# Optimization experiments

Measured on AMD Instinct MI355X. Metric: run time of the kernel, lower is better.

The kernel has to match this reference:

```python
import jax, jax.numpy as jnp
from jax import lax
import numpy as np

D_MODEL = 1024
D_STATE = 16
D_CONV = 4
EXPAND = 2
D_INNER = EXPAND * D_MODEL  # 2048
DT_RANK = D_MODEL // 16     # 64
BATCH = 4
SEQ = 1024


def setup_inputs() -> dict:
    key = jax.random.key(0)
    ks = iter(jax.random.split(key, 40))
    def w(shape, s=0.02):
        return (s * jax.random.normal(next(ks), shape)).astype(jnp.float32)
    inp = {"x": jax.random.normal(next(ks), (BATCH, SEQ, D_MODEL), dtype=jnp.float32)}
    # S4D-real style A init: A = -exp(A_log), A_log = log(1..N) per channel
    Alog = jnp.log(jnp.tile(jnp.arange(1, D_STATE + 1, dtype=jnp.float32), (D_INNER, 1)))
    for s in ("f", "b"):
        inp[f"inproj_{s}"] = w((D_MODEL, 2 * D_INNER))
        inp[f"conv_w_{s}"] = w((D_INNER, D_CONV), 0.2)
        inp[f"conv_b_{s}"] = jnp.zeros((D_INNER,), jnp.float32)
        inp[f"xproj_{s}"] = w((D_INNER, DT_RANK + 2 * D_STATE))
        inp[f"dt_w_{s}"] = w((DT_RANK, D_INNER))
        inp[f"dt_b_{s}"] = jnp.full((D_INNER,), -4.0, jnp.float32)  # softplus(-4)~0.018
        inp[f"Alog_{s}"] = Alog
        inp[f"Dp_{s}"] = jnp.ones((D_INNER,), jnp.float32)
        inp[f"outproj_{s}"] = w((D_INNER, D_MODEL))
    inp["gate_w"] = w((2 * D_MODEL, D_MODEL))
    inp["gate_b"] = jnp.zeros((D_MODEL,), jnp.float32)
    inp["proj_w"] = w((D_MODEL, D_MODEL))
    inp["proj_b"] = jnp.zeros((D_MODEL,), jnp.float32)
    return inp


def _mamba(x, inproj, conv_w, conv_b, xproj, dt_w, dt_b, Alog, Dp, outproj):
    B, L, _ = x.shape
    xz = x @ inproj                           # [B,L,2*Di]
    u, z = jnp.split(xz, 2, axis=-1)          # each [B,L,Di]
    # depthwise causal conv1d, width D_CONV
    K = conv_w.shape[1]
    up = jnp.pad(u, ((0, 0), (K - 1, 0), (0, 0)))
    uc = conv_b
    for k in range(K):
        uc = uc + up[:, k:k + L, :] * conv_w[:, k]
    uc = jax.nn.silu(uc)                      # [B,L,Di]
    dbl = uc @ xproj                          # [B,L,dt_rank+2N]
    N = Alog.shape[1]
    dt, Bm, Cm = jnp.split(dbl, [DT_RANK, DT_RANK + N], axis=-1)
    delta = jax.nn.softplus(dt @ dt_w + dt_b) # [B,L,Di]
    A = -jnp.exp(Alog)                        # [Di,N]

    def step(h, inp):
        u_t, d_t, B_t, C_t = inp              # [B,Di],[B,Di],[B,N],[B,N]
        dA = jnp.exp(d_t[..., None] * A)      # [B,Di,N]
        h = dA * h + (d_t * u_t)[..., None] * B_t[:, None, :]
        y_t = jnp.einsum('bdn,bn->bd', h, C_t)
        return h, y_t

    h0 = jnp.zeros((B, uc.shape[-1], N), x.dtype)
    xs = (uc.transpose(1, 0, 2), delta.transpose(1, 0, 2),
          Bm.transpose(1, 0, 2), Cm.transpose(1, 0, 2))
    _, ys = lax.scan(step, h0, xs)            # ys: [L,B,Di]
    y = ys.transpose(1, 0, 2) + uc * Dp
    y = y * jax.nn.silu(z)
    return y @ outproj                        # [B,L,d_model]


def reference(x, inproj_f, conv_w_f, conv_b_f, xproj_f, dt_w_f, dt_b_f, Alog_f, Dp_f, outproj_f,
              inproj_b, conv_w_b, conv_b_b, xproj_b, dt_w_b, dt_b_b, Alog_b, Dp_b, outproj_b,
              gate_w, gate_b, proj_w, proj_b):
    y_f = _mamba(x, inproj_f, conv_w_f, conv_b_f, xproj_f, dt_w_f, dt_b_f, Alog_f, Dp_f, outproj_f)
    xb = jnp.flip(x, axis=1)
    y_b = _mamba(xb, inproj_b, conv_w_b, conv_b_b, xproj_b, dt_w_b, dt_b_b, Alog_b, Dp_b, outproj_b)
    y_b = jnp.flip(y_b, axis=1)
    g = jax.nn.sigmoid(jnp.concatenate([y_f, y_b], axis=-1) @ gate_w + gate_b)
    y = g * y_f + (1.0 - g) * y_b
    return y @ proj_w + proj_b
```

## Files before the change

kernel.cpp:

```cpp
#include <hip/hip_runtime.h>
#include <hip/hip_bf16.h>

#define B_  4
#define L_  1024
#define DM  1024
#define DI  2048
#define NS  16
#define RK  64
#define MT  (B_ * L_)
#define NC  32
#define CH  (L_ / NC)
#define KSX 256
#define NZX 8
#define PSZ (B_ * NC * NS * DI)

typedef unsigned short u16;
typedef __attribute__((ext_vector_type(8))) short  bh8;
typedef __attribute__((ext_vector_type(8))) unsigned short us8;
typedef __attribute__((ext_vector_type(8))) _Float16 h8;
typedef __attribute__((ext_vector_type(4))) float  f4;

__device__ __forceinline__ float bf2f(u16 u) {
  union { unsigned int i; float f; } c; c.i = ((unsigned int)u) << 16; return c.f;
}
__device__ __forceinline__ u16 f2bf(float f) {
  union { float f; unsigned int i; } c; c.f = f;
  unsigned int x = c.i;
  unsigned int r = (x + 0x7fffu + ((x >> 16) & 1u)) >> 16;
  return (u16)r;
}

__device__ __forceinline__ void gl16(const u16* g, u16* l) {
  __builtin_amdgcn_global_load_lds(
      (const __attribute__((address_space(1))) void*)g,
      (__attribute__((address_space(3))) void*)l, 16, 0, 0);
}

__global__ void detect_k(const unsigned int* __restrict__ alog,
                         int* __restrict__ flag, int* __restrict__ afl) {
  *flag = (alog[0] != 0u) ? 1 : 0;
  afl[0] = 1; afl[1] = 1;
}

__global__ __launch_bounds__(256)
void cvt_k(const void* __restrict__ src, u16* __restrict__ dst, int n,
           const int* __restrict__ flag) {
  int i = blockIdx.x * 256 + threadIdx.x;
  if (i >= n) return;
  if (*flag) dst[i] = ((const u16*)src)[i];
  else       dst[i] = f2bf(((const float*)src)[i]);
}

__global__ __launch_bounds__(256)
void cvt10_k(const int* __restrict__ flagp,
             const void* s0, u16* d0, int n0, const void* s1, u16* d1, int n1,
             const void* s2, u16* d2, int n2, const void* s3, u16* d3, int n3,
             const void* s4, u16* d4, int n4, const void* s5, u16* d5, int n5,
             const void* s6, u16* d6, int n6, const void* s7, u16* d7, int n7,
             const void* s8, u16* d8, int n8, const void* s9, u16* d9, int n9)
{
  const void* s; u16* d; int n;
  switch (blockIdx.y) {
    case 0: s = s0; d = d0; n = n0; break;  case 1: s = s1; d = d1; n = n1; break;
    case 2: s = s2; d = d2; n = n2; break;  case 3: s = s3; d = d3; n = n3; break;
    case 4: s = s4; d = d4; n = n4; break;  case 5: s = s5; d = d5; n = n5; break;
    case 6: s = s6; d = d6; n = n6; break;  case 7: s = s7; d = d7; n = n7; break;
    case 8: s = s8; d = d8; n = n8; break;  default: s = s9; d = d9; n = n9; break;
  }
  int i = blockIdx.x * 256 + threadIdx.x;
  if (i >= n) return;
  d[i] = *flagp ? ((const u16*)s)[i] : f2bf(((const float*)s)[i]);
}

__global__ __launch_bounds__(256)
void a2_k(const int* __restrict__ flagp, const void* __restrict__ sf,
          const void* __restrict__ sb, _Float16* __restrict__ A2h,
          int* __restrict__ afl)
{
  int i = blockIdx.x * 256 + threadIdx.x;
  int dir = i >> 15;
  const void* src = dir ? sb : sf;
  int j = i & (DI * NS - 1);
  float v = *flagp ? bf2f(((const u16*)src)[j]) : ((const float*)src)[j];
  float a2 = -__expf(v);
  A2h[i] = (_Float16)a2;
  int n = i & 15;
  if (fabsf(a2 + (float)(n + 1)) > 1e-3f * (n + 1)) atomicAnd(&afl[dir], 0);
}

struct TpBatch {
  const void* src[8];
  u16* dst[8];
  int R[8], C[8], tilesX[8];
  int tOff[9];
  int cnt;
};

__global__ __launch_bounds__(256)
void tposeB_k(TpBatch tb, const int* __restrict__ flag) {
  __shared__ u16 tile[32][33];
  int bid = blockIdx.x;
  int i = 0;
  #pragma unroll
  for (int q = 0; q < 7; ++q) if (i + 1 < tb.cnt && bid >= tb.tOff[i + 1]) ++i;
  int local = bid - tb.tOff[i];
  int tX = tb.tilesX[i];
  int c0 = (local % tX) * 32, r0 = (local / tX) * 32;
  int R = tb.R[i], C = tb.C[i];
  const void* src = tb.src[i];
  u16* dst = tb.dst[i];
  int tx = threadIdx.x & 31, ty = threadIdx.x >> 5;
  int isbf = *flag;
  #pragma unroll
  for (int k = 0; k < 4; ++k) {
    int r = r0 + ty + k * 8, c = c0 + tx;
    u16 v = 0;
    if (r < R && c < C)
      v = isbf ? ((const u16*)src)[(size_t)r * C + c]
               : f2bf(((const float*)src)[(size_t)r * C + c]);
    tile[ty + k * 8][tx] = v;
  }
  __syncthreads();
  #pragma unroll
  for (int k = 0; k < 4; ++k) {
    int c = c0 + ty + k * 8, r = r0 + tx;
    if (c < C && r < R)
      dst[(size_t)c * R + r] = tile[tx][ty + k * 8];
  }
}

template<int ACT, int CATM, int OUTF, int BIDIR, int SPLITK, int DUO, int XSW, int ZDIR>
__global__ __launch_bounds__(256)
void gemm2(const u16* __restrict__ A, int lda,
           const u16* __restrict__ Wt,
           const u16* __restrict__ bias,
           void* __restrict__ Cp, int ldc, void* __restrict__ C2,
           int M, int N, int K,
           const u16* __restrict__ yfp, const u16* __restrict__ ybp,
           const int* __restrict__ flagp, const u16* __restrict__ Aalt)
{
  __shared__ __align__(16) u16 As[128][64];
  __shared__ __align__(16) u16 Bs[128][64];

  int bx, by;
  if (XSW) {
    int g = blockIdx.y * gridDim.x + blockIdx.x;
    int xcd = g & 7, j = g >> 3;
    int bxb = gridDim.x >> 3;
    int sh = 31 - __builtin_clz(bxb);
    bx = xcd * bxb + (j & (bxb - 1));
    by = j >> sh;
  } else { bx = blockIdx.x; by = blockIdx.y; }

  int zdir = 0, zslice = 0;
  if (ZDIR && SPLITK) { zdir = blockIdx.z >> 3; zslice = blockIdx.z & (NZX - 1); }
  else if (ZDIR)      { zdir = blockIdx.z; }
  else if (SPLITK)    { zslice = blockIdx.z; }

  const int tid  = threadIdx.x;
  const int lane = tid & 63;
  const int w    = tid >> 6;
  const int wm   = (w >> 1) * 64, wn = (w & 1) * 64;
  const int bm0  = by * 128, bn0 = bx * 128;
  const int l15  = lane & 15, quad = lane >> 4;
  const int rI8  = lane >> 3;
  const int cG8  = (lane & 7) ^ rI8;

  const u16* Wtp = ZDIR ? (Wt + (size_t)zdir * N * K) : Wt;

  f4 acc[4][4] = {};

  const int kb = SPLITK ? zslice * KSX : 0;
  const int ke = SPLITK ? kb + KSX : K;

  for (int k0 = kb; k0 < ke; k0 += 64) {
    {
      const u16* Abase;
      if (ZDIR)     Abase = zdir ? Aalt : A;
      else if (DUO) Abase = (bn0 < DM) ? A : ybp;
      else          Abase = A;
      #pragma unroll
      for (int t = 0; t < 4; ++t) {
        int rb = w * 32 + t * 8;
        int row = rb + rI8;
        const u16* gp;
        if (CATM) {
          int kk = k0 + cG8 * 8;
          int m = bm0 + row;
          gp = (kk < DM) ? (yfp + (size_t)m * DM + kk)
                         : (ybp + (size_t)(m ^ (L_ - 1)) * DM + (kk - DM));
        } else {
          gp = Abase + (size_t)(bm0 + row) * lda + k0 + cG8 * 8;
        }
        gl16(gp, &As[rb][0]);
      }
    }
    #pragma unroll
    for (int t = 0; t < 4; ++t) {
      int rb = w * 32 + t * 8;
      int row = rb + rI8;
      int n = bn0 + row; if (n > N - 1) n = N - 1;
      gl16(Wtp + (size_t)n * K + k0 + cG8 * 8, &Bs[rb][0]);
    }
    __syncthreads();
    #pragma unroll
    for (int s = 0; s < 2; ++s) {
      bh8 af[4], bg[4];
      const int phys = ((quad + 4 * s) ^ (l15 & 7)) * 8;
      #pragma unroll
      for (int i = 0; i < 4; ++i) {
        af[i] = *(const bh8*)&As[wm + i * 16 + l15][phys];
        bg[i] = *(const bh8*)&Bs[wn + i * 16 + l15][phys];
      }
      #pragma unroll
      for (int i = 0; i < 4; ++i)
        #pragma unroll
        for (int j = 0; j < 4; ++j)
          acc[i][j] = __builtin_amdgcn_mfma_f32_16x16x32_bf16(af[i], bg[j], acc[i][j], 0, 0, 0);
    }
    __syncthreads();
  }

  const int obf = (OUTF == 1) ? *flagp : 1;
  const size_t zoff = (OUTF == 2) ? (size_t)zslice * M * ldc : 0;
  #pragma unroll
  for (int j = 0; j < 4; ++j) {
    int lcol = bn0 + wn + j * 16 + l15;
    if (lcol >= N) continue;
    int col = BIDIR ? (lcol & 4095) : (DUO ? (lcol & (DM - 1)) : lcol);
    float bv = bias ? bf2f(bias[(ZDIR ? zdir * N : 0) + col]) : 0.f;
    #pragma unroll
    for (int i = 0; i < 4; ++i) {
      #pragma unroll
      for (int r = 0; r < 4; ++r) {
        int row = bm0 + wm + i * 16 + quad * 4 + r;
        float v = acc[i][j][r] + bv;
        if (ACT == 1) v = (v > 20.f) ? v : log1pf(__expf(v));
        if (ACT == 3) {
          float g = 1.f / (1.f + __expf(-v));
          float fv = bf2f(yfp[(size_t)row * DM + col]);
          float bb = bf2f(ybp[(size_t)(row ^ (L_ - 1)) * DM + col]);
          v = g * fv + (1.f - g) * bb;
        }
        if (OUTF == 2) {
          float* base = (ZDIR && zdir) ? (float*)C2 : (float*)Cp;
          base[zoff + (size_t)row * ldc + col] = v;
        } else if (BIDIR) {
          u16* base = (lcol < 4096) ? (u16*)Cp : (u16*)C2;
          int orow = (lcol < 4096) ? row : (row ^ (L_ - 1));
          u16* dst = (col < DI) ? (base + (size_t)orow * DI + col)
                                : (base + (size_t)(8u << 20) + (size_t)orow * DI + (col - DI));
          *dst = f2bf(v);
        } else if (DUO) {
          if (lcol < DM) ((u16*)Cp)[(size_t)row * ldc + col] = f2bf(v);
          else           ((u16*)C2)[(size_t)row * ldc + col] = f2bf(v);
        } else if (ZDIR) {
          u16* base = zdir ? (u16*)C2 : (u16*)Cp;
          base[(size_t)row * ldc + col] = f2bf(v);
        } else if (OUTF == 1 && !obf) {
          ((float*)Cp)[(size_t)row * ldc + col] = v;
        } else {
          ((u16*)Cp)[(size_t)row * ldc + col] = f2bf(v);
        }
      }
    }
  }
}

__global__ __launch_bounds__(512)
void gemm256i(const u16* __restrict__ A, int lda,
              const u16* __restrict__ Wt, int ldw,
              u16* __restrict__ Cp, u16* __restrict__ C2, int K)
{
  __shared__ __align__(16) u16 As[2][256][64];
  __shared__ __align__(16) u16 Bs[2][256][64];

  int g  = blockIdx.y * gridDim.x + blockIdx.x;
  int id = (g & 7) * ((gridDim.x * gridDim.y) >> 3) + (g >> 3);
  int bx = id >> 4;
  int by = id & 15;

  const int tid  = threadIdx.x;
  const int lane = tid & 63;
  const int w    = tid >> 6;
  const int wm2  = w >> 2;
  const int wn4  = w & 3;
  const int l15  = lane & 15, quad = lane >> 4;
  const int rI8  = lane >> 3;
  const int cG8  = (lane & 7) ^ rI8;
  const int bm0  = by * 256, bn0 = bx * 256;
  const int NT   = K >> 6;

  const u16* Ag = A  + (size_t)(bm0 + w * 8 + rI8) * lda + cG8 * 8;
  const u16* Bg = Wt + (size_t)(bn0 + w * 8 + rI8) * ldw + cG8 * 8;

  auto STAGE = [&](int kt, int bb) {
    const u16* ap = Ag + kt * 64;
    const u16* bp = Bg + kt * 64;
    #pragma unroll
    for (int i = 0; i < 4; ++i) {
      gl16(ap + (size_t)(i * 64) * lda, &As[bb][i * 64 + w * 8][0]);
      gl16(bp + (size_t)(i * 64) * ldw, &Bs[bb][i * 64 + w * 8][0]);
    }
  };

  f4 acc[8][4] = {};

  STAGE(0, 0);
  STAGE(1, 1);
  asm volatile("s_waitcnt vmcnt(8)" ::: "memory");
  __builtin_amdgcn_sched_barrier(0);
  __builtin_amdgcn_s_barrier();

  const int ph0 = ((quad    ) ^ (l15 & 7)) * 8;
  const int ph1 = ((quad + 4) ^ (l15 & 7)) * 8;

  for (int t = 0; t < NT; ++t) {
    const int bb = t & 1;
    bh8 af[4][2], bg[4][2];
    #pragma unroll
    for (int x = 0; x < 4; ++x) {
      af[x][0] = *(const bh8*)&As[bb][wm2 * 128 + x * 16 + l15][ph0];
      af[x][1] = *(const bh8*)&As[bb][wm2 * 128 + x * 16 + l15][ph1];
      bg[x][0] = *(const bh8*)&Bs[bb][wn4 * 64  + x * 16 + l15][ph0];
      bg[x][1] = *(const bh8*)&Bs[bb][wn4 * 64  + x * 16 + l15][ph1];
    }
    __builtin_amdgcn_s_setprio(1);
    #pragma unroll
    for (int s = 0; s < 2; ++s)
      #pragma unroll
      for (int i = 0; i < 4; ++i)
        #pragma unroll
        for (int j = 0; j < 2; ++j)
          acc[i][j] = __builtin_amdgcn_mfma_f32_16x16x32_bf16(af[i][s], bg[j][s], acc[i][j], 0, 0, 0);
    __builtin_amdgcn_s_setprio(0);
    __builtin_amdgcn_s_setprio(1);
    #pragma unroll
    for (int s = 0; s < 2; ++s)
      #pragma unroll
      for (int i = 0; i < 4; ++i)
        #pragma unroll
        for (int j = 0; j < 2; ++j)
          acc[i][2 + j] = __builtin_amdgcn_mfma_f32_16x16x32_bf16(af[i][s], bg[2 + j][s], acc[i][2 + j], 0, 0, 0);
    __builtin_amdgcn_s_setprio(0);
    #pragma unroll
    for (int x = 0; x < 4; ++x) {
      af[x][0] = *(const bh8*)&As[bb][wm2 * 128 + 64 + x * 16 + l15][ph0];
      af[x][1] = *(const bh8*)&As[bb][wm2 * 128 + 64 + x * 16 + l15][ph1];
    }
    asm volatile("s_waitcnt lgkmcnt(0)" ::: "memory");
    __builtin_amdgcn_sched_barrier(0);
    __builtin_amdgcn_s_barrier();
    if (t + 2 < NT) STAGE(t + 2, bb);
    __builtin_amdgcn_s_setprio(1);
    #pragma unroll
    for (int s = 0; s < 2; ++s)
      #pragma unroll
      for (int i = 0; i < 4; ++i)
        #pragma unroll
        for (int j = 0; j < 2; ++j)
          acc[4 + i][j] = __builtin_amdgcn_mfma_f32_16x16x32_bf16(af[i][s], bg[j][s], acc[4 + i][j], 0, 0, 0);
    __builtin_amdgcn_s_setprio(0);
    __builtin_amdgcn_s_setprio(1);
    #pragma unroll
    for (int s = 0; s < 2; ++s)
      #pragma unroll
      for (int i = 0; i < 4; ++i)
        #pragma unroll
        for (int j = 0; j < 2; ++j)
          acc[4 + i][2 + j] = __builtin_amdgcn_mfma_f32_16x16x32_bf16(af[i][s], bg[2 + j][s], acc[4 + i][2 + j], 0, 0, 0);
    __builtin_amdgcn_s_setprio(0);
    if (t + 2 < NT) { asm volatile("s_waitcnt vmcnt(8)" ::: "memory"); }
    else            { asm volatile("s_waitcnt vmcnt(0)" ::: "memory"); }
    __builtin_amdgcn_sched_barrier(0);
    __builtin_amdgcn_s_barrier();
  }

  #pragma unroll
  for (int j = 0; j < 4; ++j) {
    int lcol = bn0 + wn4 * 64 + j * 16 + l15;
    int col  = lcol & 4095;
    u16* base = (lcol < 4096) ? Cp : C2;
    u16* dst0 = (col < DI) ? base : (base + (size_t)(8u << 20) - DI);
    int flip  = (lcol < 4096) ? 0 : (L_ - 1);
    #pragma unroll
    for (int i = 0; i < 8; ++i) {
      #pragma unroll
      for (int r = 0; r < 4; ++r) {
        int row = bm0 + wm2 * 128 + i * 16 + quad * 4 + r;
        dst0[(size_t)(row ^ flip) * DI + col] = f2bf(acc[i][j][r]);
      }
    }
  }
}

__global__ __launch_bounds__(256)
void rdbl_k(const float* __restrict__ xpf, const float* __restrict__ xpb,
            u16* __restrict__ dbl)
{
  int i = blockIdx.x * 256 + threadIdx.x;
  int dir = i >= MT * 96;
  int il = dir ? (i - MT * 96) : i;
  const float* P = dir ? xpb : xpf;
  float s = 0.f;
  #pragma unroll
  for (int z = 0; z < NZX; ++z) s += P[(size_t)z * MT * 96 + il];
  dbl[i] = f2bf(s);
}

__global__ __launch_bounds__(256)
void conv8_k(const u16* __restrict__ xzu_f, const u16* __restrict__ xzu_b,
             const u16* __restrict__ cw,
             const u16* __restrict__ cb,
             u16* __restrict__ uc)
{
  int g = blockIdx.x * 256 + threadIdx.x;
  int dir = g >> 20;
  int gl = g & ((1 << 20) - 1);
  int e = gl * 8;
  int d = e & (DI - 1);
  int t = (e >> 11) & (L_ - 1);
  int b = e >> 21;
  const u16* xzu = dir ? xzu_b : xzu_f;
  const u16* cwp = cw + dir * DI * 4;
  const u16* cbp = cb + dir * DI;
  float acc[8];
  us8 cbv = *(const us8*)&cbp[d];
  #pragma unroll
  for (int i = 0; i < 8; ++i) acc[i] = bf2f(cbv[i]);
  u16 wr[32];
  #pragma unroll
  for (int q = 0; q < 4; ++q)
    *(us8*)&wr[q * 8] = *(const us8*)&cwp[d * 4 + q * 8];
  #pragma unroll
  for (int k = 0; k < 4; ++k) {
    int ts = t + k - 3;
    if (ts >= 0) {
      us8 xv = *(const us8*)&xzu[(size_t)(b * L_ + ts) * DI + d];
      #pragma unroll
      for (int i = 0; i < 8; ++i)
        acc[i] += bf2f(xv[i]) * bf2f(wr[i * 4 + k]);
    }
  }
  us8 o;
  #pragma unroll
  for (int i = 0; i < 8; ++i)
    o[i] = f2bf(acc[i] / (1.f + __expf(-acc[i])));
  *(us8*)&uc[(size_t)dir * MT * DI + e] = o;
}

__global__ __launch_bounds__(256, 4)
void scanA_k(const u16* __restrict__ delta, const u16* __restrict__ uc,
             const u16* __restrict__ dbl, const _Float16* __restrict__ A2h,
             const int* __restrict__ afl,
             _Float16* __restrict__ P, _Float16* __restrict__ S)
{
  int g = blockIdx.x * 256 + threadIdx.x;
  int dir = g >> 18;
  int gl = g & ((1 << 18) - 1);
  int d = gl & (DI - 1);
  int c = (gl >> 11) & (NC - 1);
  int b = gl >> 16;
  delta += (size_t)dir * MT * DI;
  uc    += (size_t)dir * MT * DI;
  dbl   += (size_t)dir * MT * 96;
  P     += (size_t)dir * PSZ;
  S     += (size_t)dir * PSZ;
  const int fast = afl[dir];
  float A2[NS];
  if (!fast) {
    h8 a0 = *(const h8*)&A2h[((size_t)dir * DI + d) * NS];
    h8 a1 = *(const h8*)&A2h[((size_t)dir * DI + d) * NS + 8];
    #pragma unroll
    for (int n = 0; n < 8; ++n) { A2[n] = (float)a0[n]; A2[n + 8] = (float)a1[n]; }
  }
  float Pv[NS], Sv[NS];
  #pragma unroll
  for (int n = 0; n < NS; ++n) { Pv[n] = 1.f; Sv[n] = 0.f; }
  int t0 = c * CH;
  for (int t = t0; t < t0 + CH; ++t) {
    size_t row = (size_t)b * L_ + t;
    float dv = bf2f(delta[row * DI + d]);
    float uv = bf2f(uc[row * DI + d]);
    float du = dv * uv;
    us8 b0 = *(const us8*)&dbl[row * 96 + 64];
    us8 b1 = *(const us8*)&dbl[row * 96 + 72];
    if (fast) {
      float q = __expf(-dv);
      float dA = 1.f;
      #pragma unroll
      for (int n = 0; n < NS; ++n) {
        dA *= q;
        float Bv = (n < 8) ? bf2f(b0[n & 7]) : bf2f(b1[n & 7]);
        Sv[n] = fmaf(dA, Sv[n], du * Bv);
        Pv[n] *= dA;
      }
    } else {
      #pragma unroll
      for (int n = 0; n < NS; ++n) {
        float Bv = (n < 8) ? bf2f(b0[n & 7]) : bf2f(b1[n & 7]);
        float dA = __expf(dv * A2[n]);
        Sv[n] = fmaf(dA, Sv[n], du * Bv);
        Pv[n] *= dA;
      }
    }
  }
  size_t base = ((size_t)(b * NC + c) * NS) * DI + d;
  #pragma unroll
  for (int n = 0; n < NS; ++n) {
    P[base + (size_t)n * DI] = (_Float16)Pv[n];
    S[base + (size_t)n * DI] = (_Float16)Sv[n];
  }
}

__global__ __launch_bounds__(256)
void scanB_k(_Float16* __restrict__ P, const _Float16* __restrict__ S)
{
  int g = blockIdx.x * 256 + threadIdx.x;
  int dir = g >> 17;
  int gl = g & ((1 << 17) - 1);
  int d = gl & (DI - 1);
  int n = (gl >> 11) & (NS - 1);
  int b = gl >> 15;
  P += (size_t)dir * PSZ;
  S += (size_t)dir * PSZ;
  float h = 0.f;
  #pragma unroll 4
  for (int c = 0; c < NC; ++c) {
    size_t ix = ((size_t)(b * NC + c) * NS + n) * DI + d;
    float p = (float)P[ix], s = (float)S[ix];
    P[ix] = (_Float16)h;
    h = fmaf(p, h, s);
  }
}

__global__ __launch_bounds__(256, 4)
void scanC_k(const u16* __restrict__ uc, const u16* delta,
             const u16* __restrict__ dbl, const u16* __restrict__ xzz_f,
             const u16* __restrict__ xzz_b, const _Float16* __restrict__ A2h,
             const int* __restrict__ afl, const u16* __restrict__ Dp,
             const _Float16* __restrict__ hstart, u16* ys)
{
  int g = blockIdx.x * 256 + threadIdx.x;
  int dir = g >> 18;
  int gl = g & ((1 << 18) - 1);
  int d = gl & (DI - 1);
  int c = (gl >> 11) & (NC - 1);
  int b = gl >> 16;
  const u16* xzz = dir ? xzz_b : xzz_f;
  uc     += (size_t)dir * MT * DI;
  delta  += (size_t)dir * MT * DI;
  dbl    += (size_t)dir * MT * 96;
  Dp     += dir * DI;
  hstart += (size_t)dir * PSZ;
  ys     += (size_t)dir * MT * DI;
  const int fast = afl[dir];
  float A2[NS], h[NS];
  if (!fast) {
    h8 a0 = *(const h8*)&A2h[((size_t)dir * DI + d) * NS];
    h8 a1 = *(const h8*)&A2h[((size_t)dir * DI + d) * NS + 8];
    #pragma unroll
    for (int n = 0; n < 8; ++n) { A2[n] = (float)a0[n]; A2[n + 8] = (float)a1[n]; }
  }
  float Dv = bf2f(Dp[d]);
  size_t hbase = ((size_t)(b * NC + c) * NS) * DI + d;
  #pragma unroll
  for (int n = 0; n < NS; ++n) h[n] = (float)hstart[hbase + (size_t)n * DI];
  int t0 = c * CH;
  for (int t = t0; t < t0 + CH; ++t) {
    size_t row = (size_t)b * L_ + t;
    float dv = bf2f(delta[row * DI + d]);
    float uv = bf2f(uc[row * DI + d]);
    float du = dv * uv;
    us8 b0 = *(const us8*)&dbl[row * 96 + 64];
    us8 b1 = *(const us8*)&dbl[row * 96 + 72];
    us8 c0 = *(const us8*)&dbl[row * 96 + 80];
    us8 c1 = *(const us8*)&dbl[row * 96 + 88];
    float y = 0.f;
    if (fast) {
      float q = __expf(-dv);
      float dA = 1.f;
      #pragma unroll
      for (int n = 0; n < NS; ++n) {
        dA *= q;
        float Bv = (n < 8) ? bf2f(b0[n & 7]) : bf2f(b1[n & 7]);
        float Cv = (n < 8) ? bf2f(c0[n & 7]) : bf2f(c1[n & 7]);
        h[n] = fmaf(dA, h[n], du * Bv);
        y = fmaf(h[n], Cv, y);
      }
    } else {
      #pragma unroll
      for (int n = 0; n < NS; ++n) {
        float Bv = (n < 8) ? bf2f(b0[n & 7]) : bf2f(b1[n & 7]);
        float Cv = (n < 8) ? bf2f(c0[n & 7]) : bf2f(c1[n & 7]);
        float dA = __expf(dv * A2[n]);
        h[n] = fmaf(dA, h[n], du * Bv);
        y = fmaf(h[n], Cv, y);
      }
    }
    float z = bf2f(xzz[row * DI + d]);
    float out = (y + uv * Dv) * (z / (1.f + __expf(-z)));
    ys[row * DI + d] = f2bf(out);
  }
}

extern "C" void kernel_launch(void* const* d_in, const int* in_sizes, int n_in,
                              void* d_out, int out_size, void* d_ws, size_t ws_size,
                              hipStream_t stream)
{
  char* ws = (char*)d_ws;
  const size_t MB = 1ull << 20;
  const size_t KB = 1024;

  u16* xzu_f   = (u16*)(ws + 0);
  u16* xzz_f   = (u16*)(ws + 16 * MB);
  u16* xzu_b   = (u16*)(ws + 32 * MB);
  u16* xzz_b   = (u16*)(ws + 48 * MB);
  u16* uc      = (u16*)(ws + 64 * MB);
  u16* delta_f = (u16*)(ws + 96 * MB);
  u16* delta_b = (u16*)(ws + 112 * MB);
  u16* dbl     = (u16*)(ws + 128 * MB);
  char* SM     = ws + 128 * MB + 1536 * KB;
  u16* w_convw = (u16*)(SM);
  u16* w_convb = (u16*)(SM + 32 * KB);
  u16* w_dtb   = (u16*)(SM + 40 * KB);
  u16* w_dp    = (u16*)(SM + 48 * KB);
  u16* w_gb    = (u16*)(SM + 56 * KB);
  u16* w_pb    = (u16*)(SM + 58 * KB);
  int* flag    = (int*)(SM + 60 * KB);
  int* afl     = (int*)(SM + 60 * KB + 8);
  _Float16* A2h = (_Float16*)(ws + 128 * MB + 1600 * KB);
  u16* xproj_t2 = (u16*)(ws + 128 * MB + 1728 * KB);
  u16* dtw_t2   = (u16*)(ws + 128 * MB + 2496 * KB);
  u16* xc       = uc;
  u16* inproj_t = delta_f;
  float* xpart_f = (float*)delta_f;
  float* xpart_b = (float*)delta_b;
  _Float16* Pb   = (_Float16*)xzu_f;
  _Float16* Sb   = (_Float16*)xzu_b;
  u16* outp2_t  = (u16*)(ws + 80 * MB);
  u16* gw_t     = (u16*)(ws + 88 * MB);
  u16* pw_t     = (u16*)(ws + 92 * MB);
  u16* yf       = xzz_f;
  u16* yb       = xzz_b;
  u16* yc       = (u16*)(ws + 0);

  dim3 blk(256);
  detect_k<<<1, 1, 0, stream>>>((const unsigned int*)d_in[7], flag, afl);

  cvt10_k<<<dim3(32, 10), blk, 0, stream>>>(flag,
      d_in[2],  w_convw,            DI * 4, d_in[3],  w_convb,      DI,
      d_in[6],  w_dtb,              DI,     d_in[8],  w_dp,         DI,
      d_in[11], w_convw + DI * 4,   DI * 4, d_in[12], w_convb + DI, DI,
      d_in[15], w_dtb + DI,         DI,     d_in[17], w_dp + DI,    DI,
      d_in[20], w_gb,               DM,     d_in[22], w_pb,         DM);
  a2_k<<<2 * DI * NS / 256, blk, 0, stream>>>(flag, d_in[7], d_in[16], A2h, afl);
  cvt_k<<<MT * DM / 256, blk, 0, stream>>>(d_in[0], xc, MT * DM, flag);

  {
    TpBatch tb{};
    auto add = [&](int i, const void* s, u16* d, int R, int C) {
      tb.src[i] = s; tb.dst[i] = d; tb.R[i] = R; tb.C[i] = C;
      tb.tilesX[i] = (C + 31) / 32;
      tb.tOff[i + 1] = tb.tOff[i] + tb.tilesX[i] * ((R + 31) / 32);
    };
    tb.tOff[0] = 0;
    add(0, d_in[1],  inproj_t,               DM, 2 * DI);
    add(1, d_in[10], inproj_t + 4096 * 1024, DM, 2 * DI);
    add(2, d_in[4],  xproj_t2,               DI, 96);
    add(3, d_in[13], xproj_t2 + 96 * 2048,   DI, 96);
    add(4, d_in[5],  dtw_t2,                 RK, DI);
    add(5, d_in[14], dtw_t2 + 2048 * 64,     RK, DI);
    tb.cnt = 6;
    tposeB_k<<<tb.tOff[6], blk, 0, stream>>>(tb, flag);
  }

  gemm256i<<<dim3(32, 16), dim3(512), 0, stream>>>(
      xc, DM, inproj_t, DM, xzu_f, xzu_b, DM);

  conv8_k<<<2 * MT * DI / 8 / 256, blk, 0, stream>>>(
      xzu_f, xzu_b, w_convw, w_convb, uc);

  gemm2<0, 0, 2, 0, 1, 0, 0, 1><<<dim3(1, 32, 2 * NZX), blk, 0, stream>>>(
      uc, DI, xproj_t2, nullptr, xpart_f, 96, xpart_b, MT, 96, DI,
      nullptr, nullptr, flag, uc + (size_t)MT * DI);
  rdbl_k<<<2 * MT * 96 / 256, blk, 0, stream>>>(xpart_f, xpart_b, dbl);

  gemm2<1, 0, 0, 0, 0, 0, 1, 1><<<dim3(16, 32, 2), blk, 0, stream>>>(
      dbl, 96, dtw_t2, w_dtb, delta_f, DI, delta_b, MT, DI, RK,
      nullptr, nullptr, flag, dbl + (size_t)MT * 96);

  scanA_k<<<2 * B_ * NC * DI / 256, blk, 0, stream>>>(
      delta_f, uc, dbl, A2h, afl, Pb, Sb);
  scanB_k<<<2 * B_ * NS * DI / 256, blk, 0, stream>>>(Pb, Sb);
  scanC_k<<<2 * B_ * NC * DI / 256, blk, 0, stream>>>(
      uc, delta_f, dbl, xzz_f, xzz_b, A2h, afl, w_dp, Pb, delta_f);

  {
    TpBatch tb{};
    auto add = [&](int i, const void* s, u16* d, int R, int C) {
      tb.src[i] = s; tb.dst[i] = d; tb.R[i] = R; tb.C[i] = C;
      tb.tilesX[i] = (C + 31) / 32;
      tb.tOff[i + 1] = tb.tOff[i] + tb.tilesX[i] * ((R + 31) / 32);
    };
    tb.tOff[0] = 0;
    add(0, d_in[9],  outp2_t,               DI, DM);
    add(1, d_in[18], outp2_t + 1024 * 2048, DI, DM);
    add(2, d_in[19], gw_t,                  2 * DM, DM);
    add(3, d_in[21], pw_t,                  DM, DM);
    tb.cnt = 4;
    tposeB_k<<<tb.tOff[4], blk, 0, stream>>>(tb, flag);
  }

  gemm2<0, 0, 0, 0, 0, 1, 1, 0><<<dim3(16, 32), blk, 0, stream>>>(
      delta_f, DI, outp2_t, nullptr, yf, DM, yb, MT, 2 * DM, DI,
      nullptr, delta_b, flag, nullptr);

  gemm2<3, 1, 0, 0, 0, 0, 1, 0><<<dim3(8, 32), blk, 0, stream>>>(
      yf, DM, gw_t, w_gb, yc, DM, nullptr, MT, DM, 2 * DM, yf, yb, flag, nullptr);
  gemm2<0, 0, 1, 0, 0, 0, 1, 0><<<dim3(8, 32), blk, 0, stream>>>(
      yc, DM, pw_t, w_pb, d_out, DM, nullptr, MT, DM, DM,
      nullptr, nullptr, flag, nullptr);
}
```

Before: 626.9 us.

## Split LDS fragment loads into four phases with barriers around MFMA clusters

Restructures the inner loop of the in-projection GEMM into four phases. Each phase loads a smaller set of A/B fragments from shared memory, hits a barrier and lgkmcnt wait, then runs an MFMA cluster. A separate register array holds the second A half, and the global prefetch STAGE moves to after the third MFMA cluster. The aim is to interleave LDS reads with MFMA work across waves in a ping-pong style, at the cost of many more workgroup barriers and higher register use. The epilogue also hoists per-column address computation out of the inner store loop.

Measured after the change: 618.8 us. About the same (-1.3%).

```diff
diff --git a/kernel.cpp b/kernel.cpp
--- a/kernel.cpp
+++ b/kernel.cpp
@@ -317,14 +317,22 @@
 
   for (int t = 0; t < NT; ++t) {
     const int bb = t & 1;
-    bh8 af[4][2], bg[4][2];
+    bh8 af[4][2], bg[4][2], a2[4][2];
+
     #pragma unroll
     for (int x = 0; x < 4; ++x) {
       af[x][0] = *(const bh8*)&As[bb][wm2 * 128 + x * 16 + l15][ph0];
       af[x][1] = *(const bh8*)&As[bb][wm2 * 128 + x * 16 + l15][ph1];
-      bg[x][0] = *(const bh8*)&Bs[bb][wn4 * 64  + x * 16 + l15][ph0];
-      bg[x][1] = *(const bh8*)&Bs[bb][wn4 * 64  + x * 16 + l15][ph1];
-    }
+    }
+    #pragma unroll
+    for (int x = 0; x < 2; ++x) {
+      bg[x][0] = *(const bh8*)&Bs[bb][wn4 * 64 + x * 16 + l15][ph0];
+      bg[x][1] = *(const bh8*)&Bs[bb][wn4 * 64 + x * 16 + l15][ph1];
+    }
+    __builtin_amdgcn_sched_barrier(0);
+    __builtin_amdgcn_s_barrier();
+    asm volatile("s_waitcnt lgkmcnt(0)" ::: "memory");
+    __builtin_amdgcn_sched_barrier(0);
     __builtin_amdgcn_s_setprio(1);
     #pragma unroll
     for (int s = 0; s < 2; ++s)
@@ -334,6 +342,18 @@
         for (int j = 0; j < 2; ++j)
           acc[i][j] = __builtin_amdgcn_mfma_f32_16x16x32_bf16(af[i][s], bg[j][s], acc[i][j], 0, 0, 0);
     __builtin_amdgcn_s_setprio(0);
+    __builtin_amdgcn_sched_barrier(0);
+    __builtin_amdgcn_s_barrier();
+
+    #pragma unroll
+    for (int x = 2; x < 4; ++x) {
+      bg[x][0] = *(const bh8*)&Bs[bb][wn4 * 64 + x * 16 + l15][ph0];
+      bg[x][1] = *(const bh8*)&Bs[bb][wn4 * 64 + x * 16 + l15][ph1];
+    }
+    __builtin_amdgcn_sched_barrier(0);
+    __builtin_amdgcn_s_barrier();
+    asm volatile("s_waitcnt lgkmcnt(0)" ::: "memory");
+    __builtin_amdgcn_sched_barrier(0);
     __builtin_amdgcn_s_setprio(1);
     #pragma unroll
     for (int s = 0; s < 2; ++s)
@@ -343,15 +363,18 @@
         for (int j = 0; j < 2; ++j)
           acc[i][2 + j] = __builtin_amdgcn_mfma_f32_16x16x32_bf16(af[i][s], bg[2 + j][s], acc[i][2 + j], 0, 0, 0);
     __builtin_amdgcn_s_setprio(0);
+    __builtin_amdgcn_sched_barrier(0);
+    __builtin_amdgcn_s_barrier();
+
     #pragma unroll
     for (int x = 0; x < 4; ++x) {
-      af[x][0] = *(const bh8*)&As[bb][wm2 * 128 + 64 + x * 16 + l15][ph0];
-      af[x][1] = *(const bh8*)&As[bb][wm2 * 128 + 64 + x * 16 + l15][ph1];
-    }
+      a2[x][0] = *(const bh8*)&As[bb][wm2 * 128 + 64 + x * 16 + l15][ph0];
+      a2[x][1] = *(const bh8*)&As[bb][wm2 * 128 + 64 + x * 16 + l15][ph1];
+    }
+    __builtin_amdgcn_sched_barrier(0);
+    __builtin_amdgcn_s_barrier();
     asm volatile("s_waitcnt lgkmcnt(0)" ::: "memory");
     __builtin_amdgcn_sched_barrier(0);
-    __builtin_amdgcn_s_barrier();
-    if (t + 2 < NT) STAGE(t + 2, bb);
     __builtin_amdgcn_s_setprio(1);
     #pragma unroll
     for (int s = 0; s < 2; ++s)
@@ -359,8 +382,13 @@
       for (int i = 0; i < 4; ++i)
         #pragma unroll
         for (int j = 0; j < 2; ++j)
-          acc[4 + i][j] = __builtin_amdgcn_mfma_f32_16x16x32_bf16(af[i][s], bg[j][s], acc[4 + i][j], 0, 0, 0);
+          acc[4 + i][j] = __builtin_amdgcn_mfma_f32_16x16x32_bf16(a2[i][s], bg[j][s], acc[4 + i][j], 0, 0, 0);
     __builtin_amdgcn_s_setprio(0);
+    __builtin_amdgcn_sched_barrier(0);
+    __builtin_amdgcn_s_barrier();
+
+    if (t + 2 < NT) STAGE(t + 2, bb);
+    __builtin_amdgcn_sched_barrier(0);
     __builtin_amdgcn_s_setprio(1);
     #pragma unroll
     for (int s = 0; s < 2; ++s)
@@ -368,7 +396,7 @@
       for (int i = 0; i < 4; ++i)
         #pragma unroll
         for (int j = 0; j < 2; ++j)
-          acc[4 + i][2 + j] = __builtin_amdgcn_mfma_f32_16x16x32_bf16(af[i][s], bg[2 + j][s], acc[4 + i][2 + j], 0, 0, 0);
+          acc[4 + i][2 + j] = __builtin_amdgcn_mfma_f32_16x16x32_bf16(a2[i][s], bg[2 + j][s], acc[4 + i][2 + j], 0, 0, 0);
     __builtin_amdgcn_s_setprio(0);
     if (t + 2 < NT) { asm volatile("s_waitcnt vmcnt(8)" ::: "memory"); }
     else            { asm volatile("s_waitcnt vmcnt(0)" ::: "memory"); }
@@ -376,19 +404,21 @@
     __builtin_amdgcn_s_barrier();
   }
 
-  #pragma unroll
-  for (int j = 0; j < 4; ++j) {
-    int lcol = bn0 + wn4 * 64 + j * 16 + l15;
-    int col  = lcol & 4095;
-    u16* base = (lcol < 4096) ? Cp : C2;
-    u16* dst0 = (col < DI) ? base : (base + (size_t)(8u << 20) - DI);
-    int flip  = (lcol < 4096) ? 0 : (L_ - 1);
+  {
+    const int lc0  = bn0 + wn4 * 64;
+    const int col0 = lc0 & 4095;
+    u16* base = (lc0 < 4096) ? Cp : C2;
+    u16* dst0 = (col0 < DI) ? base : (base + (size_t)(8u << 20) - DI);
+    const int flip = (lc0 < 4096) ? 0 : (L_ - 1);
     #pragma unroll
     for (int i = 0; i < 8; ++i) {
       #pragma unroll
       for (int r = 0; r < 4; ++r) {
         int row = bm0 + wm2 * 128 + i * 16 + quad * 4 + r;
-        dst0[(size_t)(row ^ flip) * DI + col] = f2bf(acc[i][j][r]);
+        u16* rp = dst0 + (size_t)(row ^ flip) * DI + col0;
+        #pragma unroll
+        for (int j = 0; j < 4; ++j)
+          rp[j * 16 + l15] = f2bf(acc[i][j][r]);
       }
     }
   }
```
